# Kernel tuning notes

Measured on AMD Instinct MI355X. Metric: run time of the kernel, lower is better.

## Reference

```python
import jax, jax.numpy as jnp
import numpy as np

# Izhikevich parameters (regular spiking defaults)
A = 0.02     # recovery time scale
B = 0.2      # sensitivity of recovery
C = -65.0    # reset voltage
D = 8.0      # recovery reset increment
VTH = 30.0   # spike threshold
BETA = 1.0   # surrogate gradient sharpness
DT = 0.5     # integration time step (ms)


@jax.custom_vjp
def spike_fn(v):
    # Heaviside forward, surrogate sigmoid-derivative backward
    return (v >= VTH).astype(v.dtype)

def _spike_fwd(v):
    return spike_fn(v), v

def _spike_bwd(v, g):
    s = jax.nn.sigmoid(BETA * (v - VTH))
    return (g * (BETA * s * (1.0 - s)),)

spike_fn.defvjp(_spike_fwd, _spike_bwd)


def setup_inputs() -> dict:
    key = jax.random.key(0)
    input_current = jax.random.normal(key, (32, 2000, 512), dtype=jnp.float32)
    return {"input_current": input_current}


def reference(input_current):
    # input_current: [batch, n_steps, n_neurons]
    batch, n_steps, n_neurons = input_current.shape
    dtype = input_current.dtype
    v0 = jnp.full((batch, n_neurons), C, dtype=dtype)
    u0 = jnp.full((batch, n_neurons), B * C, dtype=dtype)

    def step(carry, i_t):
        v, u = carry
        dv = (0.04 * v * v + 5.0 * v + 140.0 - u + i_t) * DT
        du = A * (B * v - u) * DT
        v = v + dv
        u = u + du
        s = spike_fn(v)
        v = v * (1.0 - s) + C * s
        u = u + D * s
        return (v, u), (s, v, u)

    xs = jnp.swapaxes(input_current, 0, 1)  # [n_steps, batch, n_neurons]
    _, (spikes, voltages, recovery) = jax.lax.scan(step, (v0, u0), xs)
    # back to [batch, n_steps, n_neurons]
    spikes = jnp.swapaxes(spikes, 0, 1)
    voltages = jnp.swapaxes(voltages, 0, 1)
    recovery = jnp.swapaxes(recovery, 0, 1)
    return spikes, voltages, recovery
```

## Files before the change

kernel.cpp:

```cpp
#include <hip/hip_runtime.h>


#define NSTEPS 2000
#define NNEUR  512
#define BATCH  32
#define INPLANE 1024000u
#define PLANE  32768000u
#define CHUNK  100
#define NCHUNK (NSTEPS / CHUNK)
#define NG     (CHUNK / 4)
#define WIN    20
#define NWIN   (CHUNK / WIN)

typedef const __attribute__((address_space(1))) unsigned GPtr;
typedef __attribute__((address_space(3))) unsigned LPtr;

__device__ __forceinline__ void izh_step(float i_t, float& v, float& u, float& s) {
#pragma clang fp contract(off)
    float t1 = 0.04f * v;
    t1 = t1 * v;
    float t2 = 5.0f * v;
    float acc = t1 + t2;
    acc = acc + 140.0f;
    acc = acc - u;
    acc = acc + i_t;
    float dv = acc * 0.5f;
    float t4 = 0.2f * v;
    t4 = t4 - u;
    t4 = 0.02f * t4;
    float du = t4 * 0.5f;
    v = v + dv;
    u = u + du;
    bool sp = (v >= 30.0f);
    s = sp ? 1.0f : 0.0f;
    v = sp ? -65.0f : v;
    u = sp ? (u + 8.0f) : u;
}

template <int W>
__device__ __forceinline__ void run_compute(const float (*lin)[CHUNK * 64],
                                            float (*ob)[WIN][64],
                                            int lane, unsigned obase,
                                            float* __restrict__ out) {
    float* oplane = out + (size_t)W * PLANE;
    float v = -65.0f;
    float u = -13.0f;
    const int r0 = lane >> 4;
    const int c4 = (lane & 15) * 4;
    int buf = 0;

    asm volatile("s_barrier" ::: "memory");
    for (int c = 0; c < NCHUNK; ++c) {
        const float* lbuf = &lin[c & 1][0];
        for (int w = 0; w < NWIN; ++w) {
            float ri[WIN];
#pragma unroll
            for (int j = 0; j < WIN; ++j) ri[j] = lbuf[(w * WIN + j) * 64 + lane];
#pragma unroll
            for (int j = 0; j < WIN; ++j) {
                float s;
                izh_step(ri[j], v, u, s);
                ob[buf][j][lane] = (W == 0) ? s : (W == 1) ? v : u;
            }
            const unsigned step0 = (unsigned)(c * CHUNK + w * WIN);
#pragma unroll
            for (int i = 0; i < WIN / 4; ++i) {
                float4 d = *(const float4*)&ob[buf][r0 + 4 * i][c4];
                size_t goff = (size_t)obase
                            + (size_t)(step0 + (unsigned)(r0 + 4 * i)) * NNEUR
                            + (size_t)(unsigned)c4;
                *(float4*)(oplane + goff) = d;
            }
            buf ^= 1;
        }
        asm volatile("s_barrier" ::: "memory");
    }
}

__global__ __launch_bounds__(256, 1) void izh_kernel(const float* __restrict__ in,
                                                     float* __restrict__ out) {
    __shared__ float lin[2][CHUNK * 64];
    __shared__ float ob[3][2][WIN][64];

    const int tid  = threadIdx.x;
    const int w    = tid >> 6;
    const int lane = tid & 63;
    const unsigned n0 = (unsigned)((blockIdx.x * 64) & (NNEUR - 1));
    const unsigned b  = (unsigned)((unsigned)(blockIdx.x * 64) >> 9);

    if (w == 3) {
        const float* gsrc = in + (size_t)b * INPLANE
                               + (size_t)(lane >> 4) * NNEUR
                               + n0 + (size_t)(lane & 15) * 4;
#pragma unroll
        for (int g = 0; g < NG; ++g) {
            __builtin_amdgcn_global_load_lds((GPtr*)(gsrc + (size_t)(4 * g) * NNEUR),
                                             (LPtr*)&lin[0][g * 256], 16, 0, 0);
        }
        asm volatile("s_waitcnt vmcnt(0)" ::: "memory");
        asm volatile("s_barrier" ::: "memory");

        for (int c = 0; c < NCHUNK; ++c) {
            if (c + 1 < NCHUNK) {
                const float* gs = gsrc + (size_t)(c + 1) * CHUNK * NNEUR;
                float* lb = &lin[(c + 1) & 1][0];
#pragma unroll
                for (int g = 0; g < NG; ++g) {
                    __builtin_amdgcn_global_load_lds((GPtr*)(gs + (size_t)(4 * g) * NNEUR),
                                                     (LPtr*)(lb + g * 256), 16, 0, 0);
                }
                asm volatile("s_waitcnt vmcnt(0)" ::: "memory");
            }
            asm volatile("s_barrier" ::: "memory");
        }
    } else {
        const unsigned obase = b * INPLANE + n0;
        if (w == 0)      run_compute<0>(lin, ob[0], lane, obase, out);
        else if (w == 1) run_compute<1>(lin, ob[1], lane, obase, out);
        else             run_compute<2>(lin, ob[2], lane, obase, out);
    }
}

extern "C" void kernel_launch(void* const* d_in, const int* in_sizes, int n_in,
                              void* d_out, int out_size, void* d_ws, size_t ws_size,
                              hipStream_t stream) {
    const float* in = (const float*)d_in[0];
    float* out = (float*)d_out;
    izh_kernel<<<(BATCH * NNEUR) / 64, 256, 0, stream>>>(in, out);
}
```

Baseline: 491.2 us.

## Swap wave roles: compute waves load inputs, dedicated wave writes outputs

Input prefetch into LDS is split across the three compute waves, while the fourth wave becomes a writer that drains a shared double-buffered output ring to global memory one window behind. Compute waves no longer issue global stores in their serial recurrence. In exchange, the block synchronizes at every window rather than every chunk, adding barrier overhead and coupling the compute waves to the writer's pace.

```diff
diff --git a/kernel.cpp b/kernel.cpp
--- a/kernel.cpp
+++ b/kernel.cpp
@@ -11,6 +11,7 @@
 #define NG     (CHUNK / 4)
 #define WIN    20
 #define NWIN   (CHUNK / WIN)
+#define NWINT  (NSTEPS / WIN)
 
 typedef const __attribute__((address_space(1))) unsigned GPtr;
 typedef __attribute__((address_space(3))) unsigned LPtr;
@@ -38,86 +39,107 @@
 }
 
 template <int W>
-__device__ __forceinline__ void run_compute(const float (*lin)[CHUNK * 64],
-                                            float (*ob)[WIN][64],
-                                            int lane, unsigned obase,
-                                            float* __restrict__ out) {
-    float* oplane = out + (size_t)W * PLANE;
+__device__ __forceinline__ void run_compute(float (*lin)[CHUNK * 64],
+                                            float (*ringP)[WIN][64],
+                                            const float* gsrc, int lane) {
+    constexpr int g0 = (W == 0) ? 0 : (W == 1) ? 8 : 16;
+    constexpr int g1 = (W == 0) ? 8 : (W == 1) ? 16 : 25;
+
+#pragma unroll
+    for (int g = g0; g < g1; ++g) {
+        __builtin_amdgcn_global_load_lds((GPtr*)(gsrc + (size_t)(4 * g) * NNEUR),
+                                         (LPtr*)(&lin[0][0] + g * 256), 16, 0, 0);
+    }
+    asm volatile("s_waitcnt vmcnt(0)" ::: "memory");
+    asm volatile("s_barrier" ::: "memory");
+
     float v = -65.0f;
     float u = -13.0f;
-    const int r0 = lane >> 4;
-    const int c4 = (lane & 15) * 4;
-    int buf = 0;
 
-    asm volatile("s_barrier" ::: "memory");
     for (int c = 0; c < NCHUNK; ++c) {
         const float* lbuf = &lin[c & 1][0];
-        for (int w = 0; w < NWIN; ++w) {
+        for (int ww = 0; ww < NWIN; ++ww) {
+            if (ww == 0 && c + 1 < NCHUNK) {
+                const float* gs = gsrc + (size_t)(c + 1) * CHUNK * NNEUR;
+                float* lb = &lin[(c + 1) & 1][0];
+#pragma unroll
+                for (int g = g0; g < g1; ++g) {
+                    __builtin_amdgcn_global_load_lds((GPtr*)(gs + (size_t)(4 * g) * NNEUR),
+                                                     (LPtr*)(lb + g * 256), 16, 0, 0);
+                }
+            }
+            const int slot = (c * NWIN + ww) & 1;
             float ri[WIN];
 #pragma unroll
-            for (int j = 0; j < WIN; ++j) ri[j] = lbuf[(w * WIN + j) * 64 + lane];
+            for (int j = 0; j < WIN; ++j) ri[j] = lbuf[(ww * WIN + j) * 64 + lane];
 #pragma unroll
             for (int j = 0; j < WIN; ++j) {
                 float s;
                 izh_step(ri[j], v, u, s);
-                ob[buf][j][lane] = (W == 0) ? s : (W == 1) ? v : u;
+                ringP[slot][j][lane] = (W == 0) ? s : (W == 1) ? v : u;
             }
-            const unsigned step0 = (unsigned)(c * CHUNK + w * WIN);
+            asm volatile("s_waitcnt lgkmcnt(0)" ::: "memory");
+            if (ww == NWIN - 1)
+                asm volatile("s_waitcnt vmcnt(0)" ::: "memory");
+            asm volatile("s_barrier" ::: "memory");
+        }
+    }
+}
+
+__device__ __forceinline__ void write_window(const float (*ring)[2][WIN][64],
+                                             int slot, unsigned wstep0,
+                                             int r0, int c4, unsigned obase,
+                                             float* __restrict__ out) {
+    float4 d[15];
 #pragma unroll
-            for (int i = 0; i < WIN / 4; ++i) {
-                float4 d = *(const float4*)&ob[buf][r0 + 4 * i][c4];
-                size_t goff = (size_t)obase
-                            + (size_t)(step0 + (unsigned)(r0 + 4 * i)) * NNEUR
-                            + (size_t)(unsigned)c4;
-                *(float4*)(oplane + goff) = d;
-            }
-            buf ^= 1;
+    for (int P = 0; P < 3; ++P)
+#pragma unroll
+        for (int i = 0; i < 5; ++i)
+            d[P * 5 + i] = *(const float4*)&ring[P][slot][r0 + 4 * i][c4];
+#pragma unroll
+    for (int P = 0; P < 3; ++P)
+#pragma unroll
+        for (int i = 0; i < 5; ++i) {
+            size_t goff = (size_t)obase
+                        + (size_t)(wstep0 + (unsigned)(r0 + 4 * i)) * NNEUR
+                        + (size_t)(unsigned)c4;
+            *(float4*)(out + (size_t)P * PLANE + goff) = d[P * 5 + i];
         }
-        asm volatile("s_barrier" ::: "memory");
-    }
 }
 
 __global__ __launch_bounds__(256, 1) void izh_kernel(const float* __restrict__ in,
                                                      float* __restrict__ out) {
     __shared__ float lin[2][CHUNK * 64];
-    __shared__ float ob[3][2][WIN][64];
+    __shared__ float ring[3][2][WIN][64];
 
     const int tid  = threadIdx.x;
     const int w    = tid >> 6;
     const int lane = tid & 63;
     const unsigned n0 = (unsigned)((blockIdx.x * 64) & (NNEUR - 1));
     const unsigned b  = (unsigned)((unsigned)(blockIdx.x * 64) >> 9);
+    const float* gsrc = in + (size_t)b * INPLANE
+                           + (size_t)(lane >> 4) * NNEUR
+                           + n0 + (size_t)(lane & 15) * 4;
 
     if (w == 3) {
-        const float* gsrc = in + (size_t)b * INPLANE
-                               + (size_t)(lane >> 4) * NNEUR
-                               + n0 + (size_t)(lane & 15) * 4;
-#pragma unroll
-        for (int g = 0; g < NG; ++g) {
-            __builtin_amdgcn_global_load_lds((GPtr*)(gsrc + (size_t)(4 * g) * NNEUR),
-                                             (LPtr*)&lin[0][g * 256], 16, 0, 0);
-        }
-        asm volatile("s_waitcnt vmcnt(0)" ::: "memory");
+        const int r0 = lane >> 4;
+        const int c4 = (lane & 15) * 4;
+        const unsigned obase = b * INPLANE + n0;
+
         asm volatile("s_barrier" ::: "memory");
-
-        for (int c = 0; c < NCHUNK; ++c) {
-            if (c + 1 < NCHUNK) {
-                const float* gs = gsrc + (size_t)(c + 1) * CHUNK * NNEUR;
-                float* lb = &lin[(c + 1) & 1][0];
-#pragma unroll
-                for (int g = 0; g < NG; ++g) {
-                    __builtin_amdgcn_global_load_lds((GPtr*)(gs + (size_t)(4 * g) * NNEUR),
-                                                     (LPtr*)(lb + g * 256), 16, 0, 0);
-                }
-                asm volatile("s_waitcnt vmcnt(0)" ::: "memory");
-            }
+        for (int gw = 0; gw < NWINT; ++gw) {
+            if (gw > 0)
+                write_window(ring, (gw - 1) & 1, (unsigned)((gw - 1) * WIN),
+                             r0, c4, obase, out);
+            asm volatile("s_waitcnt lgkmcnt(0)" ::: "memory");
             asm volatile("s_barrier" ::: "memory");
         }
+        write_window(ring, (NWINT - 1) & 1, (unsigned)((NWINT - 1) * WIN),
+                     r0, c4, obase, out);
     } else {
-        const unsigned obase = b * INPLANE + n0;
-        if (w == 0)      run_compute<0>(lin, ob[0], lane, obase, out);
-        else if (w == 1) run_compute<1>(lin, ob[1], lane, obase, out);
-        else             run_compute<2>(lin, ob[2], lane, obase, out);
+        if (w == 0)      run_compute<0>(lin, ring[0], gsrc, lane);
+        else if (w == 1) run_compute<1>(lin, ring[1], gsrc, lane);
+        else             run_compute<2>(lin, ring[2], gsrc, lane);
     }
 }
 
```

Result: slower. 505.1 us (+2.8%).
